# Optimization experiments

Measured on AMD Instinct MI355X. Metric: run time of the kernel, lower is better.

The kernel has to match this reference:

```python
import jax, jax.numpy as jnp
import numpy as np

B, N = 256, 65536          # batch, num_tokens (world.num_tokens == N)
VOCAB = 50257
ALPHA = 0.5                # dirichlet concentration
EPS = 1e-7                 # gumbel eps


def setup_inputs() -> dict:
    key = jax.random.key(0)
    kb, kt, ku, kd = jax.random.split(key, 4)
    batch = jax.random.randint(kb, (B, N), 0, VOCAB, dtype=jnp.int32)
    t = jax.random.uniform(kt, (B,), dtype=jnp.float32)
    U = jax.random.uniform(ku, (B, N), dtype=jnp.float32)
    # dirichlet(alpha=0.5) sample over the token axis, one simplex per row
    D = jax.random.dirichlet(kd, ALPHA * jnp.ones((N,), jnp.float32), shape=(B,)).astype(jnp.float32)
    return {"batch": batch, "t": t, "U": U, "D": D}


def cosine_schedule(t):
    return 1.0 - jnp.cos(jnp.pi * t / 2)


def cosine_weight(t, eps=1e-3):
    t_adj = t * (1 - 2 * eps) + eps
    return 0.5 * jnp.pi * jnp.sin(jnp.pi * t_adj / 2)


def binary_topk(weights, ks):
    # weights: [B, N] float; ks: [B, 1] int -> bool mask marking the top-k per row
    Bn, Nn = weights.shape
    idx = jnp.argsort(-weights, axis=-1)                     # descending order indices
    rank = jnp.broadcast_to(jnp.arange(Nn), (Bn, Nn))        # rank of each sorted slot
    mask = jnp.zeros((Bn, Nn), dtype=bool)
    mask = mask.at[jnp.arange(Bn)[:, None], idx].set(ks > rank)
    return mask


def reference(batch, t, U, D):
    r = cosine_schedule(t)                                   # mask rate per sample [B]
    w = cosine_weight(t)                                     # loss weight per sample [B]
    G = -jnp.log(-jnp.log(U + EPS) + EPS)                    # gumbel noise [B, N]
    weights = G + jnp.log(D)                                 # gumbel + log-dirichlet
    ks = (N * r).astype(jnp.int32)[:, None]                  # [B, 1] tokens to mask
    mask = binary_topk(weights, ks)                          # [B, N] bool
    return mask, w
```

## Files before the change

### kernel.cpp

```cpp
#include <hip/hip_runtime.h>
#include <math.h>

#define BB 256
#define NN 65536
#define NT 1024
#define CAP 2048
#define MARGIN 2e-3f

__device__ __forceinline__ unsigned int f2sort(float f) {
    unsigned int b = __float_as_uint(f);
    return (b & 0x80000000u) ? ~b : (b | 0x80000000u);
}
__device__ __forceinline__ float sort2f(unsigned int u) {
    unsigned int b = (u & 0x80000000u) ? (u & 0x7fffffffu) : ~u;
    return __uint_as_float(b);
}

__device__ __forceinline__ unsigned int wexact(float u, float d) {
    float t1 = u + 1e-7f;
    float t2 = (float)log((double)t1);
    float t3 = (-t2) + 1e-7f;
    float G  = -(float)log((double)t3);
    float lgD = (float)log((double)d);
    return f2sort(G + lgD);
}

__device__ __forceinline__ unsigned int wfast(float u, float d) {
    float t1 = u + 1e-7f;
    float t3 = -__logf(t1) + 1e-7f;
    float G  = -__logf(t3);
    return f2sort(G + __logf(d));
}

__device__ __forceinline__ bool finite_f(float f) {
    return (__float_as_uint(f) & 0x7f800000u) != 0x7f800000u;
}

#define CHUNKS(OP) OP(0) OP(1) OP(2) OP(3) OP(4) OP(5) OP(6) OP(7) \
                   OP(8) OP(9) OP(10) OP(11) OP(12) OP(13) OP(14) OP(15)

#define PASS1SEL(KKV) \
    { const int b0 = tid * 8; unsigned int cs = 0; \
      _Pragma("unroll") for (int i = 0; i < 8; i++) cs += hist[b0 + i]; \
      chunkSum[tid] = cs; } \
    __syncthreads(); \
    if (tid < 64) { \
        const int c0i = lane * 16; unsigned int s = 0; \
        _Pragma("unroll") for (int i = 0; i < 16; i++) s += chunkSum[c0i + i]; \
        unsigned int suf = s; \
        _Pragma("unroll") for (int off = 1; off < 64; off <<= 1) { \
            unsigned int tv = __shfl_down(suf, off); if (lane + off < 64) suf += tv; } \
        unsigned int above = suf - s; \
        if (suf >= (KKV) && above < (KKV)) { \
            unsigned int cum = above; \
            for (int ci = c0i + 15; ci >= c0i; ci--) { \
                unsigned int cch = chunkSum[ci]; \
                if (cum + cch >= (KKV)) { \
                    for (int b = ci * 8 + 7; ; b--) { \
                        unsigned int c2 = hist[b]; \
                        if (cum + c2 >= (KKV)) { s_sel = (unsigned int)b; s_kneed = (KKV) - cum; s_eq = c2; break; } \
                        cum += c2; } \
                    break; } \
                cum += cch; } } } \
    __syncthreads();

#define PASS2SEL(P, KN) \
    if (tid < 64) { \
        const int c0i = lane * 16; unsigned int s = 0; \
        _Pragma("unroll") for (int i = 0; i < 16; i++) s += hist[c0i + i]; \
        unsigned int suf = s; \
        _Pragma("unroll") for (int off = 1; off < 64; off <<= 1) { \
            unsigned int tv = __shfl_down(suf, off); if (lane + off < 64) suf += tv; } \
        unsigned int above = suf - s; \
        if (suf >= (KN) && above < (KN)) { \
            unsigned int cum = above; \
            for (int b = c0i + 15; ; b--) { \
                unsigned int c2 = hist[b]; \
                if (cum + c2 >= (KN)) { s_sel = ((P) << 10) | (unsigned int)b; s_kneed = (KN) - cum; s_eq = c2; break; } \
                cum += c2; } } } \
    __syncthreads();

#define PASS3SEL(P, KN) \
    if (tid < 64) { \
        const int c0i = lane * 8; unsigned int s = 0; \
        _Pragma("unroll") for (int i = 0; i < 8; i++) s += hist[c0i + i]; \
        unsigned int suf = s; \
        _Pragma("unroll") for (int off = 1; off < 64; off <<= 1) { \
            unsigned int tv = __shfl_down(suf, off); if (lane + off < 64) suf += tv; } \
        unsigned int above = suf - s; \
        if (suf >= (KN) && above < (KN)) { \
            unsigned int cum = above; \
            for (int b = c0i + 7; ; b--) { \
                unsigned int c2 = hist[b]; \
                if (cum + c2 >= (KN)) { s_sel = ((P) << 9) | (unsigned int)b; s_kneed = (KN) - cum; s_eq = c2; break; } \
                cum += c2; } } } \
    __syncthreads();

__global__ __launch_bounds__(NT) __attribute__((amdgpu_waves_per_eu(4, 4)))
void md_fused_kernel(const float* __restrict__ Tt,
                     const float* __restrict__ U,
                     const float* __restrict__ D,
                     float* __restrict__ out,
                     float* __restrict__ wout) {
    const int row = blockIdx.x;
    const int tid = threadIdx.x;
    const int lane = tid & 63;

    const float* Ur = U + (size_t)row * NN;
    const float* Dr = D + (size_t)row * NN;
    float* Or = out + (size_t)row * NN;

    __shared__ unsigned int hist[8192];
    __shared__ unsigned int chunkSum[NT];
    __shared__ unsigned int bandU[CAP];
    __shared__ int bandIdx[CAP];
    __shared__ unsigned int bitmap[2048];
    __shared__ int s_tielist[1024];
    __shared__ unsigned int s_sel, s_kneed, s_eq;
    __shared__ int s_A, s_bandCnt, s_tiecnt, s_tieidx;

    const float t = Tt[row];
    const float pf = (float)M_PI;
    float aa = pf * t;
    float bbv = aa * 0.5f;
    float c0 = (float)cos((double)bbv);
    float r  = 1.0f - c0;
    const int k = (int)(65536.0f * r);
    if (tid == 0) {
        float tadj = t * 0.998f + 0.001f;
        float arg  = (pf * tadj) * 0.5f;
        wout[row] = (float)(0.5 * M_PI) * (float)sin((double)arg);
    }

    if (k <= 0 || k >= NN) {
        const float fill = (k >= NN) ? 1.0f : 0.0f;
        float4 f4 = make_float4(fill, fill, fill, fill);
        for (int j = 0; j < 16; j++)
            *(float4*)(Or + j * 4096 + tid * 4) = f4;
        return;
    }
    const unsigned int kk = (unsigned int)k;

    uint4 v0, v1, v2, v3, v4, v5, v6, v7, v8, v9, v10, v11, v12, v13, v14, v15;

    for (int i = tid; i < 8192; i += NT) hist[i] = 0;
    if (tid == 0) { s_A = 0; s_bandCnt = 0; }
    __syncthreads();

#define COMPF(J) { \
        int e = (J) * 4096 + tid * 4; \
        float4 u4 = *(const float4*)(Ur + e); \
        float4 d4 = *(const float4*)(Dr + e); \
        v##J.x = wfast(u4.x, d4.x); \
        v##J.y = wfast(u4.y, d4.y); \
        v##J.z = wfast(u4.z, d4.z); \
        v##J.w = wfast(u4.w, d4.w); \
        atomicAdd(&hist[v##J.x >> 19], 1u); \
        atomicAdd(&hist[v##J.y >> 19], 1u); \
        atomicAdd(&hist[v##J.z >> 19], 1u); \
        atomicAdd(&hist[v##J.w >> 19], 1u); }
    CHUNKS(COMPF)
#undef COMPF
    __syncthreads();

    PASS1SEL(kk)
    const unsigned int p13 = s_sel;
    const unsigned int kn1 = s_kneed;
    hist[tid] = 0;
    __syncthreads();
#define P2F(J) { \
        if ((v##J.x >> 19) == p13) atomicAdd(&hist[(v##J.x >> 9) & 1023u], 1u); \
        if ((v##J.y >> 19) == p13) atomicAdd(&hist[(v##J.y >> 9) & 1023u], 1u); \
        if ((v##J.z >> 19) == p13) atomicAdd(&hist[(v##J.z >> 9) & 1023u], 1u); \
        if ((v##J.w >> 19) == p13) atomicAdd(&hist[(v##J.w >> 9) & 1023u], 1u); }
    CHUNKS(P2F)
#undef P2F
    __syncthreads();
    PASS2SEL(p13, kn1)

    const unsigned int p23 = s_sel;
    const float loF = sort2f(p23 << 9) - MARGIN;
    const float hiF = sort2f((p23 << 9) | 511u) + MARGIN;
    const bool badBand = !(finite_f(loF) && finite_f(hiF));
    const unsigned int lo_u = f2sort(loF);
    const unsigned int hi_u = f2sort(hiF);

    bitmap[tid] = 0;
    bitmap[tid + 1024] = 0;
    {
        int cnt = 0;
#define ACNT1(X) cnt += (int)((X) > hi_u);
#define ACNT(J) ACNT1(v##J.x) ACNT1(v##J.y) ACNT1(v##J.z) ACNT1(v##J.w)
        CHUNKS(ACNT)
#undef ACNT
#undef ACNT1
#pragma unroll
        for (int off = 32; off >= 1; off >>= 1) cnt += __shfl_down(cnt, off);
        if (lane == 0) atomicAdd(&s_A, cnt);
    }
#define GATH1(J, C, CI) { unsigned int uu = v##J.C; \
        if (uu >= lo_u && uu <= hi_u) { \
            int slot = atomicAdd(&s_bandCnt, 1); \
            if (slot < CAP) bandIdx[slot] = (J) * 4096 + tid * 4 + (CI); } }
#define GATH(J) GATH1(J, x, 0) GATH1(J, y, 1) GATH1(J, z, 2) GATH1(J, w, 3)
    CHUNKS(GATH)
#undef GATH
#undef GATH1
    __syncthreads();

    const int bandCnt = s_bandCnt;
    const int kb = k - s_A;
    const bool fallback = badBand || (bandCnt > CAP) || (kb < 0) || (kb > bandCnt);

    if (!fallback) {
        for (int j = tid; j < bandCnt; j += NT) {
            int idx = bandIdx[j];
            bandU[j] = wexact(Ur[idx], Dr[idx]);
        }
        __syncthreads();
        for (int j = tid; j < bandCnt; j += NT) {
            unsigned int me = bandU[j];
            int mi = bandIdx[j];
            int rk = 0;
            for (int i = 0; i < bandCnt; i++) {
                unsigned int o = bandU[i];
                rk += (int)((o > me) || (o == me && bandIdx[i] < mi));
            }
            if (rk < kb) atomicOr(&bitmap[mi >> 5], 1u << (mi & 31));
        }
        __syncthreads();
        const int b0 = (tid & 7) * 4;
#define WRF(J) { \
        int e = (J) * 4096 + tid * 4; \
        unsigned int wb = bitmap[(J) * 128 + (tid >> 3)]; \
        float4 m; \
        m.x = ((v##J.x > hi_u) || ((wb >> (b0 + 0)) & 1u)) ? 1.0f : 0.0f; \
        m.y = ((v##J.y > hi_u) || ((wb >> (b0 + 1)) & 1u)) ? 1.0f : 0.0f; \
        m.z = ((v##J.z > hi_u) || ((wb >> (b0 + 2)) & 1u)) ? 1.0f : 0.0f; \
        m.w = ((v##J.w > hi_u) || ((wb >> (b0 + 3)) & 1u)) ? 1.0f : 0.0f; \
        *(float4*)(Or + e) = m; }
        CHUNKS(WRF)
#undef WRF
        return;
    }

    __syncthreads();
    for (int i = tid; i < 8192; i += NT) hist[i] = 0;
    __syncthreads();
#define COMPE(J) { \
        int e = (J) * 4096 + tid * 4; \
        float4 u4 = *(const float4*)(Ur + e); \
        float4 d4 = *(const float4*)(Dr + e); \
        v##J.x = wexact(u4.x, d4.x); \
        v##J.y = wexact(u4.y, d4.y); \
        v##J.z = wexact(u4.z, d4.z); \
        v##J.w = wexact(u4.w, d4.w); \
        atomicAdd(&hist[v##J.x >> 19], 1u); \
        atomicAdd(&hist[v##J.y >> 19], 1u); \
        atomicAdd(&hist[v##J.z >> 19], 1u); \
        atomicAdd(&hist[v##J.w >> 19], 1u); }
    CHUNKS(COMPE)
#undef COMPE
    __syncthreads();

    PASS1SEL(kk)
    const unsigned int q13 = s_sel;
    const unsigned int en1 = s_kneed;
    hist[tid] = 0;
    __syncthreads();
#define P2E(J) { \
        if ((v##J.x >> 19) == q13) atomicAdd(&hist[(v##J.x >> 9) & 1023u], 1u); \
        if ((v##J.y >> 19) == q13) atomicAdd(&hist[(v##J.y >> 9) & 1023u], 1u); \
        if ((v##J.z >> 19) == q13) atomicAdd(&hist[(v##J.z >> 9) & 1023u], 1u); \
        if ((v##J.w >> 19) == q13) atomicAdd(&hist[(v##J.w >> 9) & 1023u], 1u); }
    CHUNKS(P2E)
#undef P2E
    __syncthreads();
    PASS2SEL(q13, en1)

    const unsigned int q23 = s_sel;
    const unsigned int en2 = s_kneed;
    if (tid < 512) hist[tid] = 0;
    __syncthreads();
#define P3E(J) { \
        if ((v##J.x >> 9) == q23) atomicAdd(&hist[v##J.x & 511u], 1u); \
        if ((v##J.y >> 9) == q23) atomicAdd(&hist[v##J.y & 511u], 1u); \
        if ((v##J.z >> 9) == q23) atomicAdd(&hist[v##J.z & 511u], 1u); \
        if ((v##J.w >> 9) == q23) atomicAdd(&hist[v##J.w & 511u], 1u); }
    CHUNKS(P3E)
#undef P3E
    __syncthreads();
    PASS3SEL(q23, en2)

    const unsigned int theta = s_sel;
    const unsigned int kneedF = s_kneed, eqF = s_eq;
    const bool needOrder = (kneedF < eqF);
    int istar = NN;
    if (needOrder) {
        if (tid == 0) s_tiecnt = 0;
        __syncthreads();
#define TIE1(J, C, CI) if (v##J.C == theta) { \
            int pos = atomicAdd(&s_tiecnt, 1); \
            if (pos < 1024) s_tielist[pos] = (J) * 4096 + tid * 4 + (CI); }
#define TIE(J) TIE1(J, x, 0) TIE1(J, y, 1) TIE1(J, z, 2) TIE1(J, w, 3)
        CHUNKS(TIE)
#undef TIE
#undef TIE1
        __syncthreads();
        if (tid == 0) {
            int E = s_tiecnt; if (E > 1024) E = 1024;
            for (int aI = 1; aI < E; aI++) {
                int val = s_tielist[aI]; int bI = aI - 1;
                while (bI >= 0 && s_tielist[bI] > val) { s_tielist[bI + 1] = s_tielist[bI]; bI--; }
                s_tielist[bI + 1] = val;
            }
            int kk2 = (int)kneedF; if (kk2 > E) kk2 = E; if (kk2 < 1) kk2 = 1;
            s_tieidx = s_tielist[kk2 - 1];
        }
        __syncthreads();
        istar = s_tieidx;
    }

#define MVE(u, idx) ((((u) > theta) || ((u) == theta && (!needOrder || (idx) <= istar))) ? 1.0f : 0.0f)
#define WRE(J) { \
        int e = (J) * 4096 + tid * 4; \
        float4 m; \
        m.x = MVE(v##J.x, e + 0); \
        m.y = MVE(v##J.y, e + 1); \
        m.z = MVE(v##J.z, e + 2); \
        m.w = MVE(v##J.w, e + 3); \
        *(float4*)(Or + e) = m; }
    CHUNKS(WRE)
#undef WRE
#undef MVE
}

extern "C" void kernel_launch(void* const* d_in, const int* in_sizes, int n_in,
                              void* d_out, int out_size, void* d_ws, size_t ws_size,
                              hipStream_t stream) {
    const float* T = (const float*)d_in[1];
    const float* U = (const float*)d_in[2];
    const float* D = (const float*)d_in[3];
    float* out = (float*)d_out;
    float* wout = out + (size_t)BB * NN;

    md_fused_kernel<<<BB, NT, 0, stream>>>(T, U, D, out, wout);
}
```

Before: 239.2 us.

## Fuse definite-mask write with band gather and scatter band winners directly

```diff
diff --git a/kernel.cpp b/kernel.cpp
--- a/kernel.cpp
+++ b/kernel.cpp
@@ -4,8 +4,10 @@
 #define BB 256
 #define NN 65536
 #define NT 1024
-#define CAP 2048
+#define CAP 6144
 #define MARGIN 2e-3f
+
+typedef float f32x4 __attribute__((ext_vector_type(4)));
 
 __device__ __forceinline__ unsigned int f2sort(float f) {
     unsigned int b = __float_as_uint(f);
@@ -96,7 +98,7 @@
                 cum += c2; } } } \
     __syncthreads();
 
-__global__ __launch_bounds__(NT) __attribute__((amdgpu_waves_per_eu(4, 4)))
+__global__ __launch_bounds__(NT, 4)
 void md_fused_kernel(const float* __restrict__ Tt,
                      const float* __restrict__ U,
                      const float* __restrict__ D,
@@ -114,7 +116,6 @@
     __shared__ unsigned int chunkSum[NT];
     __shared__ unsigned int bandU[CAP];
     __shared__ int bandIdx[CAP];
-    __shared__ unsigned int bitmap[2048];
     __shared__ int s_tielist[1024];
     __shared__ unsigned int s_sel, s_kneed, s_eq;
     __shared__ int s_A, s_bandCnt, s_tiecnt, s_tieidx;
@@ -134,9 +135,9 @@
 
     if (k <= 0 || k >= NN) {
         const float fill = (k >= NN) ? 1.0f : 0.0f;
-        float4 f4 = make_float4(fill, fill, fill, fill);
+        f32x4 f4 = {fill, fill, fill, fill};
         for (int j = 0; j < 16; j++)
-            *(float4*)(Or + j * 4096 + tid * 4) = f4;
+            __builtin_nontemporal_store(f4, (f32x4*)(Or + j * 4096 + tid * 4));
         return;
     }
     const unsigned int kk = (unsigned int)k;
@@ -185,27 +186,23 @@
     const unsigned int lo_u = f2sort(loF);
     const unsigned int hi_u = f2sort(hiF);
 
-    bitmap[tid] = 0;
-    bitmap[tid + 1024] = 0;
     {
         int cnt = 0;
-#define ACNT1(X) cnt += (int)((X) > hi_u);
-#define ACNT(J) ACNT1(v##J.x) ACNT1(v##J.y) ACNT1(v##J.z) ACNT1(v##J.w)
-        CHUNKS(ACNT)
-#undef ACNT
-#undef ACNT1
+#define MRG1(J, C, CI, MF) { const unsigned int uu = v##J.C; \
+        const bool din = uu > hi_u; cnt += (int)din; MF = din ? 1.0f : 0.0f; \
+        if (!din && uu >= lo_u) { \
+            int slot = atomicAdd(&s_bandCnt, 1); \
+            if (slot < CAP) bandIdx[slot] = (J) * 4096 + tid * 4 + (CI); } }
+#define MRG(J) { const int e = (J) * 4096 + tid * 4; f32x4 m; \
+        MRG1(J, x, 0, m.x) MRG1(J, y, 1, m.y) MRG1(J, z, 2, m.z) MRG1(J, w, 3, m.w) \
+        __builtin_nontemporal_store(m, (f32x4*)(Or + e)); }
+        CHUNKS(MRG)
+#undef MRG
+#undef MRG1
 #pragma unroll
         for (int off = 32; off >= 1; off >>= 1) cnt += __shfl_down(cnt, off);
         if (lane == 0) atomicAdd(&s_A, cnt);
     }
-#define GATH1(J, C, CI) { unsigned int uu = v##J.C; \
-        if (uu >= lo_u && uu <= hi_u) { \
-            int slot = atomicAdd(&s_bandCnt, 1); \
-            if (slot < CAP) bandIdx[slot] = (J) * 4096 + tid * 4 + (CI); } }
-#define GATH(J) GATH1(J, x, 0) GATH1(J, y, 1) GATH1(J, z, 2) GATH1(J, w, 3)
-    CHUNKS(GATH)
-#undef GATH
-#undef GATH1
     __syncthreads();
 
     const int bandCnt = s_bandCnt;
@@ -226,21 +223,8 @@
                 unsigned int o = bandU[i];
                 rk += (int)((o > me) || (o == me && bandIdx[i] < mi));
             }
-            if (rk < kb) atomicOr(&bitmap[mi >> 5], 1u << (mi & 31));
+            if (rk < kb) Or[mi] = 1.0f;
         }
-        __syncthreads();
-        const int b0 = (tid & 7) * 4;
-#define WRF(J) { \
-        int e = (J) * 4096 + tid * 4; \
-        unsigned int wb = bitmap[(J) * 128 + (tid >> 3)]; \
-        float4 m; \
-        m.x = ((v##J.x > hi_u) || ((wb >> (b0 + 0)) & 1u)) ? 1.0f : 0.0f; \
-        m.y = ((v##J.y > hi_u) || ((wb >> (b0 + 1)) & 1u)) ? 1.0f : 0.0f; \
-        m.z = ((v##J.z > hi_u) || ((wb >> (b0 + 2)) & 1u)) ? 1.0f : 0.0f; \
-        m.w = ((v##J.w > hi_u) || ((wb >> (b0 + 3)) & 1u)) ? 1.0f : 0.0f; \
-        *(float4*)(Or + e) = m; }
-        CHUNKS(WRF)
-#undef WRF
         return;
     }
 
@@ -324,12 +308,12 @@
 #define MVE(u, idx) ((((u) > theta) || ((u) == theta && (!needOrder || (idx) <= istar))) ? 1.0f : 0.0f)
 #define WRE(J) { \
         int e = (J) * 4096 + tid * 4; \
-        float4 m; \
+        f32x4 m; \
         m.x = MVE(v##J.x, e + 0); \
         m.y = MVE(v##J.y, e + 1); \
         m.z = MVE(v##J.z, e + 2); \
         m.w = MVE(v##J.w, e + 3); \
-        *(float4*)(Or + e) = m; }
+        __builtin_nontemporal_store(m, (f32x4*)(Or + e)); }
     CHUNKS(WRE)
 #undef WRE
 #undef MVE
```

New measurement: 231.7 us. 1.03x faster.
